# Kernel optimization log

Hardware: AMD Instinct MI355X
Metric: run time of the kernel (lower is better)

The kernel has to match this reference:

```python
import jax, jax.numpy as jnp
import numpy as np

N = 25000      # nodes
E = 400000     # edges (before self loops)
G = 64         # graphs in batch
H = 16         # attention heads
ITER = 10      # stacked main GATv2 layers


def setup_inputs():
    key = jax.random.key(0)
    c = [0]
    def nk():
        c[0] += 1
        return jax.random.fold_in(key, c[0])
    def glorot(shape):
        fan = shape[-2] + shape[-1]
        return jax.random.normal(nk(), shape, jnp.float32) * np.float32(np.sqrt(2.0 / fan))
    inp = {
        "x": jax.random.normal(nk(), (N, 2), jnp.float32),
        "edge_attr": jax.random.normal(nk(), (E, 2), jnp.float32),
        "edge_index": jax.random.randint(nk(), (2, E), 0, N, jnp.int32),
        "mask": jax.random.randint(nk(), (N,), 0, 2, jnp.int32),
        "batch": jnp.sort(jax.random.randint(nk(), (N,), 0, G, jnp.int32)),
        # gcn: GATv2Conv(2, 4, heads=16, edge_dim=2), concat -> 64
        "g0_Wl": glorot((2, 64)), "g0_bl": jnp.zeros((64,), jnp.float32),
        "g0_Wr": glorot((2, 64)), "g0_br": jnp.zeros((64,), jnp.float32),
        "g0_We": glorot((2, 64)), "g0_att": glorot((H, 4)),
        "g0_bias": jnp.zeros((64,), jnp.float32),
        "bn_gamma": jnp.ones((64,), jnp.float32),
        "bn_beta": jnp.zeros((64,), jnp.float32),
        "m_Wl": glorot((ITER, 64, 64)), "m_bl": jnp.zeros((ITER, 64), jnp.float32),
        "m_Wr": glorot((ITER, 64, 64)), "m_br": jnp.zeros((ITER, 64), jnp.float32),
        "m_We": glorot((ITER, 2, 64)), "m_att": glorot((ITER, H, 4)),
        "m_bias": jnp.zeros((ITER, 64), jnp.float32),
        # final: GATv2Conv(64, 1, heads=16, concat=False)
        "f_Wl": glorot((64, 16)), "f_bl": jnp.zeros((16,), jnp.float32),
        "f_Wr": glorot((64, 16)), "f_br": jnp.zeros((16,), jnp.float32),
        "f_We": glorot((2, 16)), "f_att": glorot((H, 1)),
        "f_bias": jnp.zeros((1,), jnp.float32),
        # sbs: GATv2Conv(64, 1, heads=16, concat=False)
        "s_Wl": glorot((64, 16)), "s_bl": jnp.zeros((16,), jnp.float32),
        "s_Wr": glorot((64, 16)), "s_br": jnp.zeros((16,), jnp.float32),
        "s_We": glorot((2, 16)), "s_att": glorot((H, 1)),
        "s_bias": jnp.zeros((1,), jnp.float32),
    }
    return inp


def _gatv2(x, src, dst, eattr, Wl, bl, Wr, br, We, att, bias, concat):
    """PyG GATv2Conv: x_l[j]+x_r[i]+e -> LeakyReLU(0.2) -> att dot -> segment softmax over dst."""
    n = x.shape[0]
    h, c = att.shape
    xl = (x @ Wl + bl).reshape(n, h, c)
    xr = (x @ Wr + br).reshape(n, h, c)
    e = (eattr @ We).reshape(-1, h, c)
    m = jax.nn.leaky_relu(xl[src] + xr[dst] + e, 0.2)          # [Etot,H,C]
    logit = jnp.einsum('ehc,hc->eh', m, att)                    # [Etot,H]
    lmax = jax.ops.segment_max(logit, dst, num_segments=n)
    ex = jnp.exp(logit - lmax[dst])
    den = jax.ops.segment_sum(ex, dst, num_segments=n)
    alpha = ex / den[dst]
    out = jax.ops.segment_sum(xl[src] * alpha[..., None], dst, num_segments=n)  # [N,H,C]
    out = out.reshape(n, h * c) if concat else out.mean(axis=1)
    return out + bias


def reference(x, edge_attr, edge_index, mask, batch,
              g0_Wl, g0_bl, g0_Wr, g0_br, g0_We, g0_att, g0_bias,
              bn_gamma, bn_beta,
              m_Wl, m_bl, m_Wr, m_br, m_We, m_att, m_bias,
              f_Wl, f_bl, f_Wr, f_br, f_We, f_att, f_bias,
              s_Wl, s_bl, s_Wr, s_br, s_We, s_att, s_bias):
    n = x.shape[0]
    src, dst = edge_index[0], edge_index[1]
    # add self loops; self-loop edge attr = mean of incoming edge attrs (fill_value='mean')
    ones = jnp.ones((src.shape[0],), jnp.float32)
    cnt = jax.ops.segment_sum(ones, dst, num_segments=n)
    esum = jax.ops.segment_sum(edge_attr, dst, num_segments=n)
    loop_attr = esum / jnp.maximum(cnt, 1.0)[:, None]
    arng = jnp.arange(n, dtype=edge_index.dtype)
    src2 = jnp.concatenate([src, arng])
    dst2 = jnp.concatenate([dst, arng])
    ea2 = jnp.concatenate([edge_attr, loop_attr], axis=0)

    h0 = _gatv2(x, src2, dst2, ea2, g0_Wl, g0_bl, g0_Wr, g0_br, g0_We, g0_att, g0_bias, True)
    mu = h0.mean(axis=0)
    var = h0.var(axis=0)
    h = jax.nn.leaky_relu((h0 - mu) * jax.lax.rsqrt(var + 1e-5) * bn_gamma + bn_beta, 0.01)

    def step(hc, p):
        Wl, bl, Wr, br, We, att, bias = p
        hc = jax.nn.leaky_relu(_gatv2(hc, src2, dst2, ea2, Wl, bl, Wr, br, We, att, bias, True), 0.01)
        return hc, None
    h, _ = jax.lax.scan(step, h, (m_Wl, m_bl, m_Wr, m_br, m_We, m_att, m_bias))

    mus = _gatv2(h, src2, dst2, ea2, s_Wl, s_bl, s_Wr, s_br, s_We, s_att, s_bias, False)[:, 0]  # [N]
    fin = _gatv2(h, src2, dst2, ea2, f_Wl, f_bl, f_Wr, f_br, f_We, f_att, f_bias, False)        # [N,1]
    w = (mask == 0).astype(jnp.float32)
    sums = jax.ops.segment_sum(fin * w[:, None], batch, num_segments=G)
    cnts = jax.ops.segment_sum(w, batch, num_segments=G)
    sat = (sums / jnp.maximum(cnts, 1.0)[:, None])[:, 0]  # [G]
    return mus, sat
```

## Files before the change

kernel.cpp:

```cpp
#include <hip/hip_runtime.h>


static __device__ __forceinline__ float lrelu(float x, float s) {
    return x > 0.f ? x : s * x;
}

__global__ void k_build0(const int* __restrict__ dst, int* __restrict__ cnt,
                         int* __restrict__ rank, int E,
                         const float* __restrict__ x,
                         const float* __restrict__ Wl, const float* __restrict__ bl,
                         const float* __restrict__ Wr, const float* __restrict__ br,
                         float* __restrict__ xl, float* __restrict__ xr, int n) {
    int idx = blockIdx.x * blockDim.x + threadIdx.x;
    if (idx < E) {
        rank[idx] = atomicAdd(&cnt[dst[idx]], 1);
    } else {
        int t = idx - E;
        if (t < n * 64) {
            int i = t >> 6, c = t & 63;
            float x0 = x[2 * i], x1 = x[2 * i + 1];
            xl[t] = x0 * Wl[c] + x1 * Wl[64 + c] + bl[c];
            xr[t] = x0 * Wr[c] + x1 * Wr[64 + c] + br[c];
        }
    }
}

__global__ void k_segoff(const int* __restrict__ cnt, int* __restrict__ row_start,
                         int* __restrict__ cursor, int n) {
    int i = blockIdx.x * blockDim.x + threadIdx.x;
    int lane = threadIdx.x & 63;
    int v = (i < n) ? cnt[i] + 1 : 0;
    int s = v;
#pragma unroll
    for (int off = 1; off < 64; off <<= 1) {
        int t = __shfl_up(s, off);
        if (lane >= off) s += t;
    }
    int wavetot = __shfl(s, 63);
    int base = 0;
    if (lane == 63) base = atomicAdd(cursor, wavetot);
    base = __shfl(base, 63);
    if (i < n) row_start[i] = base + s - v;
}

__global__ void k_scatter(const int* __restrict__ src, const int* __restrict__ dst,
                          const float* __restrict__ ea, const int* __restrict__ rank,
                          const int* __restrict__ row_start,
                          int* __restrict__ csr_src, float* __restrict__ csr_ea, int E) {
    int e = blockIdx.x * blockDim.x + threadIdx.x;
    if (e >= E) return;
    int pos = row_start[dst[e]] + rank[e];
    csr_src[pos] = src[e];
    *(float2*)(csr_ea + 2 * (size_t)pos) = *(const float2*)(ea + 2 * (size_t)e);
}

__global__ void k_selfloop(const int* __restrict__ row_start, const int* __restrict__ cnt,
                           int* __restrict__ csr_src, float* __restrict__ csr_ea, int n) {
    int i = blockIdx.x * blockDim.x + threadIdx.x;
    if (i >= n) return;
    int p0 = row_start[i], deg = cnt[i];
    float s0 = 0.f, s1 = 0.f;
    for (int p = p0; p < p0 + deg; ++p) {
        s0 += csr_ea[2 * (size_t)p];
        s1 += csr_ea[2 * (size_t)p + 1];
    }
    float c = fmaxf((float)deg, 1.f);
    int pl = p0 + deg;
    csr_src[pl] = i;
    csr_ea[2 * (size_t)pl] = s0 / c;
    csr_ea[2 * (size_t)pl + 1] = s1 / c;
}

__launch_bounds__(256)
__global__ void k_proj64(const float* __restrict__ h,
                         const float* __restrict__ Wl, const float* __restrict__ bl,
                         const float* __restrict__ Wr, const float* __restrict__ br,
                         const double* __restrict__ stats,
                         const float* __restrict__ bng, const float* __restrict__ bnb,
                         float* __restrict__ xl, float* __restrict__ xr, int n) {
    __shared__ float wsl[4096], wsr[4096], bna[64], bnbb[64];
    int t = threadIdx.x;
    for (int i = t; i < 4096; i += 256) { wsl[i] = Wl[i]; wsr[i] = Wr[i]; }
    if (t < 64) {
        double mu = stats[t] / n;
        double var = stats[64 + t] / n - mu * mu;
        float rs = (float)(1.0 / sqrt(var + 1e-5));
        float a = rs * bng[t];
        bna[t] = a;
        bnbb[t] = bnb[t] - (float)mu * a;
    }
    __syncthreads();
    int rg = t >> 2, cg4 = (t & 3) << 4;
    int r0 = blockIdx.x * 128 + rg * 2;
    float accl[2][16], accr[2][16];
#pragma unroll
    for (int r = 0; r < 2; ++r)
#pragma unroll
        for (int j = 0; j < 16; ++j) { accl[r][j] = 0.f; accr[r][j] = 0.f; }
    for (int k0 = 0; k0 < 64; k0 += 4) {
        float hk[2][4];
#pragma unroll
        for (int r = 0; r < 2; ++r) {
            int gr = r0 + r;
            float4 v = (gr < n) ? *(const float4*)(h + (size_t)gr * 64 + k0)
                                : make_float4(0.f, 0.f, 0.f, 0.f);
            hk[r][0] = v.x; hk[r][1] = v.y; hk[r][2] = v.z; hk[r][3] = v.w;
#pragma unroll
            for (int kk = 0; kk < 4; ++kk)
                hk[r][kk] = lrelu(hk[r][kk] * bna[k0 + kk] + bnbb[k0 + kk], 0.01f);
        }
#pragma unroll
        for (int kk = 0; kk < 4; ++kk) {
            const float* wl = wsl + (k0 + kk) * 64 + cg4;
            const float* wr = wsr + (k0 + kk) * 64 + cg4;
#pragma unroll
            for (int r = 0; r < 2; ++r)
#pragma unroll
                for (int j = 0; j < 16; ++j) {
                    accl[r][j] += hk[r][kk] * wl[j];
                    accr[r][j] += hk[r][kk] * wr[j];
                }
        }
    }
#pragma unroll
    for (int r = 0; r < 2; ++r) {
        int gr = r0 + r;
        if (gr < n) {
            float* ol = xl + (size_t)gr * 64 + cg4;
            float* orr = xr + (size_t)gr * 64 + cg4;
#pragma unroll
            for (int j = 0; j < 16; ++j) {
                ol[j] = accl[r][j] + bl[cg4 + j];
                orr[j] = accr[r][j] + br[cg4 + j];
            }
        }
    }
}

__device__ __forceinline__ float gat_node(const float* __restrict__ xl,
                                          const float* __restrict__ xr,
                                          const int* __restrict__ row_start,
                                          const int* __restrict__ cnt,
                                          const int* __restrict__ csr_src,
                                          const float* __restrict__ csr_ea,
                                          const float* __restrict__ We,
                                          const float* __restrict__ att,
                                          const float* __restrict__ bias,
                                          int d, int lane, int relu) {
    const int p0 = __builtin_amdgcn_readfirstlane(row_start[d]);
    const int p1 = p0 + __builtin_amdgcn_readfirstlane(cnt[d]) + 1;
    const float we0 = We[lane], we1 = We[64 + lane];
    const float av = att[lane];
    const float xrv = xr[(size_t)d * 64 + lane];

    float den0 = 0.f, acc0 = 0.f;
    float den1 = 0.f, acc1 = 0.f;

    auto step = [&](float xv, float2 ea, bool valid, float& den, float& acc) {
        float tv = lrelu(xv + xrv + ea.x * we0 + ea.y * we1, 0.2f) * av;
        tv += __shfl_xor(tv, 1);
        tv += __shfl_xor(tv, 2);
        if (!valid) tv = -__builtin_inff();
        float w = __expf(tv);
        den += w;
        acc += w * xv;
    };

    for (int p = p0; p < p1; p += 4) {
        int q1 = min(p + 1, p1 - 1), q2 = min(p + 2, p1 - 1), q3 = min(p + 3, p1 - 1);
        int s0 = csr_src[p], s1 = csr_src[q1], s2 = csr_src[q2], s3 = csr_src[q3];
        float2 e0 = *(const float2*)(csr_ea + 2 * (size_t)p);
        float2 e1 = *(const float2*)(csr_ea + 2 * (size_t)q1);
        float2 e2 = *(const float2*)(csr_ea + 2 * (size_t)q2);
        float2 e3 = *(const float2*)(csr_ea + 2 * (size_t)q3);
        float x0 = xl[(size_t)s0 * 64 + lane];
        float x1 = xl[(size_t)s1 * 64 + lane];
        float x2 = xl[(size_t)s2 * 64 + lane];
        float x3 = xl[(size_t)s3 * 64 + lane];
        step(x0, e0, true, den0, acc0);
        step(x1, e1, p + 1 < p1, den1, acc1);
        step(x2, e2, p + 2 < p1, den0, acc0);
        step(x3, e3, p + 3 < p1, den1, acc1);
    }
    float o = (acc0 + acc1) / (den0 + den1) + bias[lane];
    if (relu) o = lrelu(o, 0.01f);
    return o;
}

__launch_bounds__(256)
__global__ void k_gat(const float* __restrict__ xl, const float* __restrict__ xr,
                      const int* __restrict__ row_start, const int* __restrict__ cnt,
                      const int* __restrict__ csr_src, const float* __restrict__ csr_ea,
                      const float* __restrict__ We, const float* __restrict__ att,
                      const float* __restrict__ bias,
                      float* __restrict__ out, int n, int relu) {
    int wave = (blockIdx.x * blockDim.x + threadIdx.x) >> 6;
    int lane = threadIdx.x & 63;
    if (wave >= n) return;
    float o = gat_node(xl, xr, row_start, cnt, csr_src, csr_ea, We, att, bias, wave, lane, relu);
    out[(size_t)wave * 64 + lane] = o;
}

__launch_bounds__(256)
__global__ void k_gat_proj(const float* __restrict__ xl, const float* __restrict__ xr,
                           const int* __restrict__ row_start, const int* __restrict__ cnt,
                           const int* __restrict__ csr_src, const float* __restrict__ csr_ea,
                           const float* __restrict__ We, const float* __restrict__ att,
                           const float* __restrict__ bias,
                           const float* __restrict__ Wnl, const float* __restrict__ bnl,
                           const float* __restrict__ Wnr, const float* __restrict__ bnr,
                           float* __restrict__ xl_out, float* __restrict__ xr_out, int n) {
    int wave = (blockIdx.x * blockDim.x + threadIdx.x) >> 6;
    int lane = threadIdx.x & 63;
    if (wave >= n) return;
    const int d = wave;
    float o = gat_node(xl, xr, row_start, cnt, csr_src, csr_ea, We, att, bias, d, lane, 1);
    float a0 = 0.f, a1 = 0.f, b0 = 0.f, b1 = 0.f;
#pragma unroll 8
    for (int k = 0; k < 64; k += 2) {
        float h0 = __shfl(o, k);
        float h1 = __shfl(o, k + 1);
        a0 += h0 * Wnl[k * 64 + lane];
        a1 += h1 * Wnl[(k + 1) * 64 + lane];
        b0 += h0 * Wnr[k * 64 + lane];
        b1 += h1 * Wnr[(k + 1) * 64 + lane];
    }
    xl_out[(size_t)d * 64 + lane] = a0 + a1 + bnl[lane];
    xr_out[(size_t)d * 64 + lane] = b0 + b1 + bnr[lane];
}

__launch_bounds__(256)
__global__ void k_gat_projfin(const float* __restrict__ xl, const float* __restrict__ xr,
                              const int* __restrict__ row_start, const int* __restrict__ cnt,
                              const int* __restrict__ csr_src, const float* __restrict__ csr_ea,
                              const float* __restrict__ We, const float* __restrict__ att,
                              const float* __restrict__ bias,
                              const float* __restrict__ fWl, const float* __restrict__ fbl,
                              const float* __restrict__ fWr, const float* __restrict__ fbr,
                              const float* __restrict__ sWl, const float* __restrict__ sbl,
                              const float* __restrict__ sWr, const float* __restrict__ sbr,
                              float* __restrict__ packed, int n) {
    int wave = (blockIdx.x * blockDim.x + threadIdx.x) >> 6;
    int lane = threadIdx.x & 63;
    if (wave >= n) return;
    const int d = wave;
    float o = gat_node(xl, xr, row_start, cnt, csr_src, csr_ea, We, att, bias, d, lane, 1);
    int q = lane >> 4, cc = lane & 15;
    const float* W = (q == 0) ? fWl : (q == 1) ? sWl : (q == 2) ? fWr : sWr;
    const float* B = (q == 0) ? fbl : (q == 1) ? sbl : (q == 2) ? fbr : sbr;
    float a0 = 0.f, a1 = 0.f;
#pragma unroll 8
    for (int k = 0; k < 64; k += 2) {
        a0 += __shfl(o, k) * W[k * 16 + cc];
        a1 += __shfl(o, k + 1) * W[(k + 1) * 16 + cc];
    }
    packed[(size_t)d * 64 + lane] = a0 + a1 + B[cc];
}

__launch_bounds__(256)
__global__ void k_gat_final(const float* __restrict__ packed,
                            const int* __restrict__ row_start, const int* __restrict__ cnt,
                            const int* __restrict__ csr_src, const float* __restrict__ csr_ea,
                            const float* __restrict__ fWe, const float* __restrict__ sWe,
                            const float* __restrict__ fatt, const float* __restrict__ satt,
                            const float* __restrict__ fbias, const float* __restrict__ sbias,
                            float* __restrict__ fin, float* __restrict__ mus, int n) {
    int hw = (blockIdx.x * blockDim.x + threadIdx.x) >> 5;
    if (hw >= n) return;
    int l = threadIdx.x & 31;
    int hh = l & 15, sel = l >> 4;
    const int d = hw;
    const int p0 = row_start[d], p1 = p0 + cnt[d] + 1;
    const float* We = sel ? sWe : fWe;
    float we0 = We[hh], we1 = We[16 + hh];
    float av = (sel ? satt : fatt)[hh];
    float xrv = packed[(size_t)d * 64 + 32 + sel * 16 + hh];
    int xli = sel * 16 + hh;

    float den0 = 0.f, acc0 = 0.f;
    float den1 = 0.f, acc1 = 0.f;

    auto step = [&](float xv, float2 ea, bool valid, float& den, float& acc) {
        float t = lrelu(xv + xrv + ea.x * we0 + ea.y * we1, 0.2f) * av;
        if (!valid) t = -__builtin_inff();
        float w = __expf(t);
        den += w;
        acc += w * xv;
    };

    for (int p = p0; p < p1; p += 4) {
        int q1 = min(p + 1, p1 - 1), q2 = min(p + 2, p1 - 1), q3 = min(p + 3, p1 - 1);
        int s0 = csr_src[p], s1 = csr_src[q1], s2 = csr_src[q2], s3 = csr_src[q3];
        float2 e0 = *(const float2*)(csr_ea + 2 * (size_t)p);
        float2 e1 = *(const float2*)(csr_ea + 2 * (size_t)q1);
        float2 e2 = *(const float2*)(csr_ea + 2 * (size_t)q2);
        float2 e3 = *(const float2*)(csr_ea + 2 * (size_t)q3);
        float x0 = packed[(size_t)s0 * 64 + xli];
        float x1 = packed[(size_t)s1 * 64 + xli];
        float x2 = packed[(size_t)s2 * 64 + xli];
        float x3 = packed[(size_t)s3 * 64 + xli];
        step(x0, e0, true, den0, acc0);
        step(x1, e1, p + 1 < p1, den1, acc1);
        step(x2, e2, p + 2 < p1, den0, acc0);
        step(x3, e3, p + 3 < p1, den1, acc1);
    }
    float val = (acc0 + acc1) / (den0 + den1);
#pragma unroll
    for (int w = 1; w < 16; w <<= 1) val += __shfl_xor(val, w);
    if ((threadIdx.x & 15) == 0) {
        float o = val * (1.f / 16.f) + (sel ? sbias[0] : fbias[0]);
        if (sel) mus[d] = o; else fin[d] = o;
    }
}


__global__ void k_bnstats(const float* __restrict__ h, double* __restrict__ stats, int n) {
    int c = threadIdx.x & 63;
    int s0 = blockIdx.x * (blockDim.x >> 6) + (threadIdx.x >> 6);
    int ns = gridDim.x * (blockDim.x >> 6);
    double s = 0.0, s2 = 0.0;
    for (int i = s0; i < n; i += ns) {
        float v = h[(size_t)i * 64 + c];
        s += v;
        s2 += (double)v * v;
    }
    atomicAdd(&stats[c], s);
    atomicAdd(&stats[64 + c], s2);
}


__global__ void k_sat_acc(const float* __restrict__ fin, const int* __restrict__ mask,
                          const int* __restrict__ batch,
                          float* __restrict__ sums, float* __restrict__ cnts, int n) {
    int i = blockIdx.x * blockDim.x + threadIdx.x;
    int lane = threadIdx.x & 63;
    int g = (i < n) ? batch[i] : -1;
    float c = (i < n && mask[i] == 0) ? 1.f : 0.f;
    float v = (c > 0.f) ? fin[i] : 0.f;
#pragma unroll
    for (int off = 1; off < 64; off <<= 1) {
        float v2 = __shfl_down(v, off);
        float c2 = __shfl_down(c, off);
        int g2 = __shfl_down(g, off);
        if (lane + off < 64 && g2 == g) { v += v2; c += c2; }
    }
    int gprev = __shfl_up(g, 1);
    bool head = (lane == 0) || (gprev != g);
    if (head && g >= 0 && c > 0.f) {
        atomicAdd(&sums[g], v);
        atomicAdd(&cnts[g], c);
    }
}

__global__ void k_sat_fin(const float* __restrict__ sums, const float* __restrict__ cnts,
                          float* __restrict__ out, int g) {
    int i = threadIdx.x;
    if (i < g) out[i] = sums[i] / fmaxf(cnts[i], 1.f);
}


extern "C" void kernel_launch(void* const* d_in, const int* in_sizes, int n_in,
                              void* d_out, int out_size, void* d_ws, size_t ws_size,
                              hipStream_t stream) {
    const float* x = (const float*)d_in[0];
    const float* eat = (const float*)d_in[1];
    const int* ei = (const int*)d_in[2];
    const int* mask = (const int*)d_in[3];
    const int* batch = (const int*)d_in[4];
    const float* g0_Wl = (const float*)d_in[5];
    const float* g0_bl = (const float*)d_in[6];
    const float* g0_Wr = (const float*)d_in[7];
    const float* g0_br = (const float*)d_in[8];
    const float* g0_We = (const float*)d_in[9];
    const float* g0_att = (const float*)d_in[10];
    const float* g0_bias = (const float*)d_in[11];
    const float* bn_g = (const float*)d_in[12];
    const float* bn_b = (const float*)d_in[13];
    const float* m_Wl = (const float*)d_in[14];
    const float* m_bl = (const float*)d_in[15];
    const float* m_Wr = (const float*)d_in[16];
    const float* m_br = (const float*)d_in[17];
    const float* m_We = (const float*)d_in[18];
    const float* m_att = (const float*)d_in[19];
    const float* m_bias = (const float*)d_in[20];
    const float* f_Wl = (const float*)d_in[21];
    const float* f_bl = (const float*)d_in[22];
    const float* f_Wr = (const float*)d_in[23];
    const float* f_br = (const float*)d_in[24];
    const float* f_We = (const float*)d_in[25];
    const float* f_att = (const float*)d_in[26];
    const float* f_bias = (const float*)d_in[27];
    const float* s_Wl = (const float*)d_in[28];
    const float* s_bl = (const float*)d_in[29];
    const float* s_Wr = (const float*)d_in[30];
    const float* s_br = (const float*)d_in[31];
    const float* s_We = (const float*)d_in[32];
    const float* s_att = (const float*)d_in[33];
    const float* s_bias = (const float*)d_in[34];

    const int N = in_sizes[3];
    const int E = in_sizes[1] / 2;
    const int G = out_size - N;
    const int ITER = in_sizes[14] / 4096;
    const int ET = E + N;
    const int* srcp = ei;
    const int* dstp = ei + E;

    char* wsb = (char*)d_ws;
    size_t off = 0;
    auto alloc = [&](size_t b) { void* p = wsb + off; off = (off + b + 255) & ~(size_t)255; return p; };
    int* cnt = (int*)alloc((size_t)N * 4);
    int* cursor = (int*)alloc(256);
    double* stats = (double*)alloc(128 * 8);
    float* sums = (float*)alloc((size_t)G * 4);
    float* cnts = (float*)alloc((size_t)G * 4);
    size_t zero_bytes = off;
    int* rank = (int*)alloc((size_t)E * 4);
    int* row_start = (int*)alloc((size_t)N * 4);
    int* csr_src = (int*)alloc((size_t)ET * 4);
    float* csr_ea = (float*)alloc((size_t)ET * 8);
    float* xlA = (float*)alloc((size_t)N * 256);
    float* xrA = (float*)alloc((size_t)N * 256);
    float* xlB = (float*)alloc((size_t)N * 256);
    float* xrB = (float*)alloc((size_t)N * 256);
    float* hbuf = (float*)alloc((size_t)N * 256);
    float* fin = (float*)alloc((size_t)N * 4);
    (void)ws_size; (void)n_in;

    float* outv = (float*)d_out;

    hipMemsetAsync(d_ws, 0, zero_bytes, stream);
    const int tb = 256;
    const int ggrid = (N * 64 + 255) / 256;
    k_build0<<<(E + N * 64 + tb - 1) / tb, tb, 0, stream>>>(dstp, cnt, rank, E,
                                                            x, g0_Wl, g0_bl, g0_Wr, g0_br,
                                                            xlA, xrA, N);
    k_segoff<<<(N + tb - 1) / tb, tb, 0, stream>>>(cnt, row_start, cursor, N);
    k_scatter<<<(E + tb - 1) / tb, tb, 0, stream>>>(srcp, dstp, eat, rank, row_start,
                                                    csr_src, csr_ea, E);
    k_selfloop<<<(N + tb - 1) / tb, tb, 0, stream>>>(row_start, cnt, csr_src, csr_ea, N);

    k_gat<<<ggrid, tb, 0, stream>>>(xlA, xrA, row_start, cnt, csr_src, csr_ea,
                                    g0_We, g0_att, g0_bias, hbuf, N, 0);
    k_bnstats<<<128, 256, 0, stream>>>(hbuf, stats, N);
    k_proj64<<<(N + 127) / 128, 256, 0, stream>>>(hbuf, m_Wl, m_bl, m_Wr, m_br,
                                                  stats, bn_g, bn_b, xlA, xrA, N);

    float* cur_l = xlA; float* cur_r = xrA;
    float* alt_l = xlB; float* alt_r = xrB;
    for (int l = 0; l < ITER; ++l) {
        if (l < ITER - 1) {
            k_gat_proj<<<ggrid, tb, 0, stream>>>(cur_l, cur_r, row_start, cnt, csr_src, csr_ea,
                                                 m_We + l * 128, m_att + l * 64, m_bias + l * 64,
                                                 m_Wl + (size_t)(l + 1) * 4096, m_bl + (l + 1) * 64,
                                                 m_Wr + (size_t)(l + 1) * 4096, m_br + (l + 1) * 64,
                                                 alt_l, alt_r, N);
        } else {
            k_gat_projfin<<<ggrid, tb, 0, stream>>>(cur_l, cur_r, row_start, cnt, csr_src, csr_ea,
                                                    m_We + l * 128, m_att + l * 64, m_bias + l * 64,
                                                    f_Wl, f_bl, f_Wr, f_br,
                                                    s_Wl, s_bl, s_Wr, s_br,
                                                    alt_l, N);
        }
        float* t;
        t = cur_l; cur_l = alt_l; alt_l = t;
        t = cur_r; cur_r = alt_r; alt_r = t;
    }
    k_gat_final<<<(N * 32 + tb - 1) / tb, tb, 0, stream>>>(cur_l, row_start, cnt, csr_src, csr_ea,
                                                           f_We, s_We, f_att, s_att,
                                                           f_bias, s_bias, fin, outv, N);
    k_sat_acc<<<(N + tb - 1) / tb, tb, 0, stream>>>(fin, mask, batch, sums, cnts, N);
    k_sat_fin<<<1, 64, 0, stream>>>(sums, cnts, outv + N, G);
}
```

Measured before the change: 649.3 us.

## Schedule GAT node waves in degree-sorted order via counting-sort permutation

Adds a histogram, bin-offset scan and permutation pass that orders nodes by in-degree, highest first. Every GAT kernel then maps each wave or half-wave to the node perm[wave] rather than to the wave index. The aim is to cut load imbalance and tail effects from the random degree distribution by starting the long rows first and grouping rows of similar length into the same blocks. In exchange there are three extra small launches, one indirection per wave, and node order no longer matches memory order, which can hurt locality of the output writes and of the row_start/cnt reads.

```diff
diff --git a/kernel.cpp b/kernel.cpp
--- a/kernel.cpp
+++ b/kernel.cpp
@@ -43,6 +43,36 @@
     if (i < n) row_start[i] = base + s - v;
 }
 
+__global__ void k_hist(const int* __restrict__ cnt, int* __restrict__ hist, int n) {
+    int i = blockIdx.x * blockDim.x + threadIdx.x;
+    if (i < n) atomicAdd(&hist[min(cnt[i], 127)], 1);
+}
+
+__global__ void k_binoff(int* __restrict__ hist) {
+    int l = threadIdx.x & 63;
+    int b0 = 127 - 2 * l, b1 = 126 - 2 * l;
+    int h0 = hist[b0], h1 = hist[b1];
+    int s = h0 + h1;
+    int ex = s;
+#pragma unroll
+    for (int off = 1; off < 64; off <<= 1) {
+        int t = __shfl_up(ex, off);
+        if (l >= off) ex += t;
+    }
+    int base = ex - s;
+    hist[b0] = base;
+    hist[b1] = base + h0;
+}
+
+__global__ void k_perm(const int* __restrict__ cnt, int* __restrict__ hist,
+                       int* __restrict__ perm, int n) {
+    int i = blockIdx.x * blockDim.x + threadIdx.x;
+    if (i >= n) return;
+    int b = min(cnt[i], 127);
+    int pos = atomicAdd(&hist[b], 1);
+    perm[pos] = i;
+}
+
 __global__ void k_scatter(const int* __restrict__ src, const int* __restrict__ dst,
                           const float* __restrict__ ea, const int* __restrict__ rank,
                           const int* __restrict__ row_start,
@@ -191,29 +221,32 @@
 __global__ void k_gat(const float* __restrict__ xl, const float* __restrict__ xr,
                       const int* __restrict__ row_start, const int* __restrict__ cnt,
                       const int* __restrict__ csr_src, const float* __restrict__ csr_ea,
+                      const int* __restrict__ perm,
                       const float* __restrict__ We, const float* __restrict__ att,
                       const float* __restrict__ bias,
                       float* __restrict__ out, int n, int relu) {
-    int wave = (blockIdx.x * blockDim.x + threadIdx.x) >> 6;
+    int wv = (blockIdx.x * blockDim.x + threadIdx.x) >> 6;
     int lane = threadIdx.x & 63;
-    if (wave >= n) return;
-    float o = gat_node(xl, xr, row_start, cnt, csr_src, csr_ea, We, att, bias, wave, lane, relu);
-    out[(size_t)wave * 64 + lane] = o;
+    if (wv >= n) return;
+    int d = __builtin_amdgcn_readfirstlane(perm[wv]);
+    float o = gat_node(xl, xr, row_start, cnt, csr_src, csr_ea, We, att, bias, d, lane, relu);
+    out[(size_t)d * 64 + lane] = o;
 }
 
 __launch_bounds__(256)
 __global__ void k_gat_proj(const float* __restrict__ xl, const float* __restrict__ xr,
                            const int* __restrict__ row_start, const int* __restrict__ cnt,
                            const int* __restrict__ csr_src, const float* __restrict__ csr_ea,
+                           const int* __restrict__ perm,
                            const float* __restrict__ We, const float* __restrict__ att,
                            const float* __restrict__ bias,
                            const float* __restrict__ Wnl, const float* __restrict__ bnl,
                            const float* __restrict__ Wnr, const float* __restrict__ bnr,
                            float* __restrict__ xl_out, float* __restrict__ xr_out, int n) {
-    int wave = (blockIdx.x * blockDim.x + threadIdx.x) >> 6;
+    int wv = (blockIdx.x * blockDim.x + threadIdx.x) >> 6;
     int lane = threadIdx.x & 63;
-    if (wave >= n) return;
-    const int d = wave;
+    if (wv >= n) return;
+    const int d = __builtin_amdgcn_readfirstlane(perm[wv]);
     float o = gat_node(xl, xr, row_start, cnt, csr_src, csr_ea, We, att, bias, d, lane, 1);
     float a0 = 0.f, a1 = 0.f, b0 = 0.f, b1 = 0.f;
 #pragma unroll 8
@@ -233,6 +266,7 @@
 __global__ void k_gat_projfin(const float* __restrict__ xl, const float* __restrict__ xr,
                               const int* __restrict__ row_start, const int* __restrict__ cnt,
                               const int* __restrict__ csr_src, const float* __restrict__ csr_ea,
+                              const int* __restrict__ perm,
                               const float* __restrict__ We, const float* __restrict__ att,
                               const float* __restrict__ bias,
                               const float* __restrict__ fWl, const float* __restrict__ fbl,
@@ -240,10 +274,10 @@
                               const float* __restrict__ sWl, const float* __restrict__ sbl,
                               const float* __restrict__ sWr, const float* __restrict__ sbr,
                               float* __restrict__ packed, int n) {
-    int wave = (blockIdx.x * blockDim.x + threadIdx.x) >> 6;
+    int wv = (blockIdx.x * blockDim.x + threadIdx.x) >> 6;
     int lane = threadIdx.x & 63;
-    if (wave >= n) return;
-    const int d = wave;
+    if (wv >= n) return;
+    const int d = __builtin_amdgcn_readfirstlane(perm[wv]);
     float o = gat_node(xl, xr, row_start, cnt, csr_src, csr_ea, We, att, bias, d, lane, 1);
     int q = lane >> 4, cc = lane & 15;
     const float* W = (q == 0) ? fWl : (q == 1) ? sWl : (q == 2) ? fWr : sWr;
@@ -261,6 +295,7 @@
 __global__ void k_gat_final(const float* __restrict__ packed,
                             const int* __restrict__ row_start, const int* __restrict__ cnt,
                             const int* __restrict__ csr_src, const float* __restrict__ csr_ea,
+                            const int* __restrict__ perm,
                             const float* __restrict__ fWe, const float* __restrict__ sWe,
                             const float* __restrict__ fatt, const float* __restrict__ satt,
                             const float* __restrict__ fbias, const float* __restrict__ sbias,
@@ -269,7 +304,7 @@
     if (hw >= n) return;
     int l = threadIdx.x & 31;
     int hh = l & 15, sel = l >> 4;
-    const int d = hw;
+    const int d = perm[hw];
     const int p0 = row_start[d], p1 = p0 + cnt[d] + 1;
     const float* We = sel ? sWe : fWe;
     float we0 = We[hh], we1 = We[16 + hh];
@@ -411,12 +446,14 @@
     auto alloc = [&](size_t b) { void* p = wsb + off; off = (off + b + 255) & ~(size_t)255; return p; };
     int* cnt = (int*)alloc((size_t)N * 4);
     int* cursor = (int*)alloc(256);
+    int* hist = (int*)alloc(128 * 4);
     double* stats = (double*)alloc(128 * 8);
     float* sums = (float*)alloc((size_t)G * 4);
     float* cnts = (float*)alloc((size_t)G * 4);
     size_t zero_bytes = off;
     int* rank = (int*)alloc((size_t)E * 4);
     int* row_start = (int*)alloc((size_t)N * 4);
+    int* perm = (int*)alloc((size_t)N * 4);
     int* csr_src = (int*)alloc((size_t)ET * 4);
     float* csr_ea = (float*)alloc((size_t)ET * 8);
     float* xlA = (float*)alloc((size_t)N * 256);
@@ -436,11 +473,14 @@
                                                             x, g0_Wl, g0_bl, g0_Wr, g0_br,
                                                             xlA, xrA, N);
     k_segoff<<<(N + tb - 1) / tb, tb, 0, stream>>>(cnt, row_start, cursor, N);
+    k_hist<<<(N + tb - 1) / tb, tb, 0, stream>>>(cnt, hist, N);
+    k_binoff<<<1, 64, 0, stream>>>(hist);
+    k_perm<<<(N + tb - 1) / tb, tb, 0, stream>>>(cnt, hist, perm, N);
     k_scatter<<<(E + tb - 1) / tb, tb, 0, stream>>>(srcp, dstp, eat, rank, row_start,
                                                     csr_src, csr_ea, E);
     k_selfloop<<<(N + tb - 1) / tb, tb, 0, stream>>>(row_start, cnt, csr_src, csr_ea, N);
 
-    k_gat<<<ggrid, tb, 0, stream>>>(xlA, xrA, row_start, cnt, csr_src, csr_ea,
+    k_gat<<<ggrid, tb, 0, stream>>>(xlA, xrA, row_start, cnt, csr_src, csr_ea, perm,
                                     g0_We, g0_att, g0_bias, hbuf, N, 0);
     k_bnstats<<<128, 256, 0, stream>>>(hbuf, stats, N);
     k_proj64<<<(N + 127) / 128, 256, 0, stream>>>(hbuf, m_Wl, m_bl, m_Wr, m_br,
@@ -451,12 +491,14 @@
     for (int l = 0; l < ITER; ++l) {
         if (l < ITER - 1) {
             k_gat_proj<<<ggrid, tb, 0, stream>>>(cur_l, cur_r, row_start, cnt, csr_src, csr_ea,
+                                                 perm,
                                                  m_We + l * 128, m_att + l * 64, m_bias + l * 64,
                                                  m_Wl + (size_t)(l + 1) * 4096, m_bl + (l + 1) * 64,
                                                  m_Wr + (size_t)(l + 1) * 4096, m_br + (l + 1) * 64,
                                                  alt_l, alt_r, N);
         } else {
             k_gat_projfin<<<ggrid, tb, 0, stream>>>(cur_l, cur_r, row_start, cnt, csr_src, csr_ea,
+                                                    perm,
                                                     m_We + l * 128, m_att + l * 64, m_bias + l * 64,
                                                     f_Wl, f_bl, f_Wr, f_br,
                                                     s_Wl, s_bl, s_Wr, s_br,
@@ -467,6 +509,7 @@
         t = cur_r; cur_r = alt_r; alt_r = t;
     }
     k_gat_final<<<(N * 32 + tb - 1) / tb, tb, 0, stream>>>(cur_l, row_start, cnt, csr_src, csr_ea,
+                                                           perm,
                                                            f_We, s_We, f_att, s_att,
                                                            f_bias, s_bias, fin, outv, N);
     k_sat_acc<<<(N + tb - 1) / tb, tb, 0, stream>>>(fin, mask, batch, sums, cnts, N);
```

Result: slower. 784.9 us (+20.9%).
